# Performance work log

Measured on AMD Instinct MI355X. Metric: run time of the kernel, lower is better.

The kernel has to match this reference:

```python
import jax, jax.numpy as jnp
import numpy as np

B, M, T, L, K = 64, 16, 2048, 64, 32
N = T - L + 1  # 1985 sliding-window positions


def setup_inputs() -> dict:
    key = jax.random.key(0)
    k1, k2, k3 = jax.random.split(key, 3)
    x = jax.random.normal(k1, (B, M, T), dtype=jnp.float32)
    # shapelets initialized uniform(-1, 1) as in nn.init.uniform_
    shapelets = jax.random.uniform(k2, (K, L), dtype=jnp.float32, minval=-1.0, maxval=1.0)
    # penalty maps (learned; zeros at init, random here for a non-trivial weighting)
    penalty_maps = 0.1 * jax.random.normal(k3, (K, M, N), dtype=jnp.float32)
    return {"x": x, "shapelets": shapelets, "penalty_maps": penalty_maps}


def reference(x, shapelets, penalty_maps):
    # x: (B, M, T); shapelets: (K, L); penalty_maps: (K, M, N)
    Lw = shapelets.shape[1]
    n_pos = x.shape[2] - Lw + 1
    # sliding-window view: (B, M, N, L), equivalent to torch unfold(dim=2, size=L, step=1)
    idx = jnp.arange(n_pos)[:, None] + jnp.arange(Lw)[None, :]
    sub = x[:, :, idx]  # (B, M, N, L)

    def per_shapelet(args):
        shp, pmap = args  # (L,), (M, N)
        # raw squared L2 distance over window, per channel/position: (B, M, N)
        raw = jnp.sum((sub - shp[None, None, None, :]) ** 2, axis=3)
        pen = jax.nn.elu(-pmap) + 2.0  # (M, N)
        wd = jnp.sum(raw * pen[None], axis=1)  # sum over channels -> (B, N)
        return jnp.min(wd, axis=1)  # min over positions -> (B,)

    # sequential map over the K shapelets avoids a Kx blow-up of the (B,M,N,L) intermediate
    feats = jax.lax.map(per_shapelet, (shapelets, penalty_maps))  # (K, B)
    return feats.T  # (B, K)
```

## Files before the change

kernel.cpp:

```cpp
#include <hip/hip_runtime.h>
#include <hip/hip_bf16.h>

#define B_ 64
#define M_ 16
#define T_ 2048
#define L_ 64
#define K_ 32
#define N_ (T_ - L_ + 1)
#define KMN (K_ * M_ * N_)
#define TN 64
#define NTH 256
#define XROW 128
#define STSTR 72
#define SQSTR 68

typedef __attribute__((ext_vector_type(8))) short bf16x8;
typedef __attribute__((ext_vector_type(4))) float f32x4;

__device__ __forceinline__ unsigned short f2bf(float f) {
    __hip_bfloat16 h = __float2bfloat16(f);
    return __builtin_bit_cast(unsigned short, h);
}

__device__ __forceinline__ unsigned funnel16(unsigned lo, unsigned hi, unsigned sh) {
    return (unsigned)(((((unsigned long long)hi) << 32) | lo) >> sh);
}

__device__ __forceinline__ bf16x8 extract_frag(uint4 a, uint4 b, unsigned sh, int c2) {
    unsigned t0 = funnel16(a.x, a.y, sh), t1 = funnel16(a.y, a.z, sh);
    unsigned t2 = funnel16(a.z, a.w, sh), t3 = funnel16(a.w, b.x, sh);
    unsigned t4 = funnel16(b.x, b.y, sh), t5 = funnel16(b.y, b.z, sh);
    unsigned t6 = funnel16(b.z, b.w, sh);
    const bool s2 = (c2 & 2), s1 = (c2 & 1);
    unsigned u0 = s2 ? t2 : t0, u1 = s2 ? t3 : t1, u2 = s2 ? t4 : t2;
    unsigned u3 = s2 ? t5 : t3, u4 = s2 ? t6 : t4;
    union { unsigned u[4]; bf16x8 v; } cvt;
    cvt.u[0] = s1 ? u1 : u0; cvt.u[1] = s1 ? u2 : u1;
    cvt.u[2] = s1 ? u3 : u2; cvt.u[3] = s1 ? u4 : u3;
    return cvt.v;
}

__global__ void pen_init_kernel(const float* __restrict__ pmap,
                                float* __restrict__ pen,
                                unsigned* __restrict__ out) {
    const int gid = blockIdx.x * 256 + threadIdx.x;
    if (gid < B_ * K_) out[gid] = 0x7F800000u;
    if (gid < KMN / 4) {
        const int i4 = gid * 4;
        float4 p = *(const float4*)(pmap + i4);
        float4 r;
        r.x = (p.x < 0.f) ? (2.f - p.x) : (__expf(-p.x) + 1.f);
        r.y = (p.y < 0.f) ? (2.f - p.y) : (__expf(-p.y) + 1.f);
        r.z = (p.z < 0.f) ? (2.f - p.z) : (__expf(-p.z) + 1.f);
        r.w = (p.w < 0.f) ? (2.f - p.w) : (__expf(-p.w) + 1.f);
        *(float4*)(pen + i4) = r;
    }
}

__global__ __launch_bounds__(NTH, 2)
void shapelet_mfma_kernel(const float* __restrict__ x,
                          const float* __restrict__ shp,
                          const float* __restrict__ pen,
                          unsigned* __restrict__ out) {
    __shared__ __align__(16) unsigned short xbuf[M_][XROW];
    __shared__ __align__(16) unsigned short st[K_][STSTR];
    __shared__ __align__(16) float sqw[M_][SQSTR];
    __shared__ float ss_l[K_];

    const int tid = threadIdx.x;
    const int n0 = blockIdx.x * TN;
    const int b  = blockIdx.y;
    const bool fast = (n0 + TN < T_);

    const float* xb = x + ((size_t)b * M_) * T_ + n0;
    for (int g = tid; g < M_ * 32; g += NTH) {
        const int m = g >> 5, j4 = (g & 31) * 4;
        const float* src = xb + m * T_ + j4;
        float4 v;
        if (fast) {
            v = *(const float4*)src;
        } else {
            v = make_float4(0.f, 0.f, 0.f, 0.f);
            const int t = n0 + j4;
            if (t     < T_) v.x = src[0];
            if (t + 1 < T_) v.y = src[1];
            if (t + 2 < T_) v.z = src[2];
            if (t + 3 < T_) v.w = src[3];
        }
        ushort4 sv = { f2bf(v.x), f2bf(v.y), f2bf(v.z), f2bf(v.w) };
        *(ushort4*)&xbuf[m][j4] = sv;
    }
    for (int i = tid; i < K_ * 16; i += NTH) {
        const int k = i >> 4, l4 = (i & 15) * 4;
        float4 v = *(const float4*)(shp + k * L_ + l4);
        ushort4 sv = { f2bf(v.x), f2bf(v.y), f2bf(v.z), f2bf(v.w) };
        *(ushort4*)&st[k][l4] = sv;
    }
    if (tid < K_) {
        float s = 0.f;
        for (int l = 0; l < L_; ++l) { float v = shp[tid * L_ + l]; s = fmaf(v, v, s); }
        ss_l[tid] = s;
    }
    if (tid < M_ * 8) {
        const int m = tid >> 3, j0 = (tid & 7) * 8;
        const float* xr = x + ((size_t)b * M_ + m) * T_ + n0;
        float s = 0.f;
        if (fast) {
#pragma unroll
            for (int qd = 0; qd < 16; ++qd) {
                float4 v = *(const float4*)(xr + j0 + qd * 4);
                s = fmaf(v.x, v.x, s); s = fmaf(v.y, v.y, s);
                s = fmaf(v.z, v.z, s); s = fmaf(v.w, v.w, s);
            }
            sqw[m][j0] = s;
#pragma unroll
            for (int d = 1; d < 8; ++d) {
                float a = xr[j0 + d + L_ - 1], r = xr[j0 + d - 1];
                s += a * a - r * r;
                sqw[m][j0 + d] = s;
            }
        } else {
            for (int l = 0; l < L_; ++l) {
                float v = (n0 + j0 + l < T_) ? xr[j0 + l] : 0.f;
                s = fmaf(v, v, s);
            }
            sqw[m][j0] = s;
            for (int d = 1; d < 8; ++d) {
                float a = (n0 + j0 + d + L_ - 1 < T_) ? xr[j0 + d + L_ - 1] : 0.f;
                float r = (n0 + j0 + d - 1 < T_) ? xr[j0 + d - 1] : 0.f;
                s += a * a - r * r;
                sqw[m][j0 + d] = s;
            }
        }
    }
    __syncthreads();

    const int lane = tid & 63;
    const int w  = tid >> 6;
    const int rl = lane & 15;
    const int q  = lane >> 4;
    const int rho = rl & 7, r8 = rl >> 3;
    const unsigned sh = (unsigned)((rho & 1) * 16);
    const int c2 = rho >> 1;
    const int Gb = 2 * w + q + r8;

    bf16x8 bfr[2][2];
#pragma unroll
    for (int t = 0; t < 2; ++t)
#pragma unroll
        for (int h = 0; h < 2; ++h)
            bfr[t][h] = *(const bf16x8*)&st[16 * t + rl][8 * q + 32 * h];

    const float ssk0 = ss_l[rl], ssk1 = ss_l[16 + rl];

    f32x4 wd0 = (f32x4)0.f, wd1 = (f32x4)0.f;
    const int nrow = n0 + 16 * w + 4 * q;
    const f32x4 zero = (f32x4)0.f;

#pragma unroll 2
    for (int m = 0; m < M_; ++m) {
        float4 p0, p1;
        const float* pr0 = pen + ((size_t)(rl * M_ + m)) * N_ + nrow;
        const float* pr1 = pen + ((size_t)((16 + rl) * M_ + m)) * N_ + nrow;
        if (fast) {
            p0 = *(const float4*)pr0;
            p1 = *(const float4*)pr1;
        } else {
            p0 = make_float4(2.f, 2.f, 2.f, 2.f);
            p1 = make_float4(2.f, 2.f, 2.f, 2.f);
            if (nrow     < N_) { p0.x = pr0[0]; p1.x = pr1[0]; }
            if (nrow + 1 < N_) { p0.y = pr0[1]; p1.y = pr1[1]; }
            if (nrow + 2 < N_) { p0.z = pr0[2]; p1.z = pr1[2]; }
            if (nrow + 3 < N_) { p0.w = pr0[3]; p1.w = pr1[3]; }
        }

        const uint4* px = (const uint4*)&xbuf[m][0];
        uint4 w0 = px[Gb],     w1 = px[Gb + 1];
        uint4 w2 = px[Gb + 4], w3 = px[Gb + 5];
        bf16x8 a0 = extract_frag(w0, w1, sh, c2);
        bf16x8 a1 = extract_frag(w2, w3, sh, c2);

        f32x4 corr0 = __builtin_amdgcn_mfma_f32_16x16x32_bf16(a0, bfr[0][0], zero, 0, 0, 0);
        corr0       = __builtin_amdgcn_mfma_f32_16x16x32_bf16(a1, bfr[0][1], corr0, 0, 0, 0);
        f32x4 corr1 = __builtin_amdgcn_mfma_f32_16x16x32_bf16(a0, bfr[1][0], zero, 0, 0, 0);
        corr1       = __builtin_amdgcn_mfma_f32_16x16x32_bf16(a1, bfr[1][1], corr1, 0, 0, 0);

        f32x4 sq = *(const f32x4*)&sqw[m][16 * w + 4 * q];
        const float pe0[4] = { p0.x, p0.y, p0.z, p0.w };
        const float pe1[4] = { p1.x, p1.y, p1.z, p1.w };
#pragma unroll
        for (int r = 0; r < 4; ++r) {
            float t0v = fmaf(-2.f, corr0[r], sq[r] + ssk0);
            wd0[r] = fmaf(pe0[r], t0v, wd0[r]);
            float t1v = fmaf(-2.f, corr1[r], sq[r] + ssk1);
            wd1[r] = fmaf(pe1[r], t1v, wd1[r]);
        }
    }

#pragma unroll
    for (int t = 0; t < 2; ++t) {
        float lmin = __int_as_float(0x7F800000);
        const f32x4& wdv = t ? wd1 : wd0;
#pragma unroll
        for (int r = 0; r < 4; ++r) {
            if (nrow + r < N_) lmin = fminf(lmin, wdv[r]);
        }
        lmin = fminf(lmin, __shfl_xor(lmin, 16));
        lmin = fminf(lmin, __shfl_xor(lmin, 32));
        if (q == 0) {
            atomicMin(out + (size_t)b * K_ + 16 * t + rl,
                      __float_as_uint(fmaxf(lmin, 0.f)));
        }
    }
}

extern "C" void kernel_launch(void* const* d_in, const int* in_sizes, int n_in,
                              void* d_out, int out_size, void* d_ws, size_t ws_size,
                              hipStream_t stream) {
    const float* x    = (const float*)d_in[0];
    const float* shp  = (const float*)d_in[1];
    const float* pmap = (const float*)d_in[2];
    unsigned* out = (unsigned*)d_out;
    float* pen = (float*)d_ws;

    pen_init_kernel<<<dim3((KMN / 4 + 255) / 256), dim3(256), 0, stream>>>(pmap, pen, out);

    dim3 grid((N_ + TN - 1) / TN, B_);
    shapelet_mfma_kernel<<<grid, dim3(NTH), 0, stream>>>(x, shp, pen, out);
}
```

Baseline: 106.0 us.

## Prefetch penalty loads ahead, precompute shapelet norms, reduce atomics via shared memory

Penalty-map loads are software-pipelined, with two channel iterations prefetched into registers ahead of compute. The first loads are issued before the staging phase so global latency overlaps the x/shapelet conversion. Shapelet squared norms move into the init kernel and are stored in workspace instead of being computed serially by 32 threads in every block. Per-wave minima are combined in shared memory so each block issues 32 atomics instead of 128. The cost is more register pressure from the prefetch buffers and one extra barrier.

```diff
diff --git a/kernel.cpp b/kernel.cpp
--- a/kernel.cpp
+++ b/kernel.cpp
@@ -41,10 +41,17 @@
 }
 
 __global__ void pen_init_kernel(const float* __restrict__ pmap,
+                                const float* __restrict__ shp,
                                 float* __restrict__ pen,
+                                float* __restrict__ ss_ws,
                                 unsigned* __restrict__ out) {
     const int gid = blockIdx.x * 256 + threadIdx.x;
     if (gid < B_ * K_) out[gid] = 0x7F800000u;
+    if (gid < K_) {
+        float s = 0.f;
+        for (int l = 0; l < L_; ++l) { float v = shp[gid * L_ + l]; s = fmaf(v, v, s); }
+        ss_ws[gid] = s;
+    }
     if (gid < KMN / 4) {
         const int i4 = gid * 4;
         float4 p = *(const float4*)(pmap + i4);
@@ -61,16 +68,53 @@
 void shapelet_mfma_kernel(const float* __restrict__ x,
                           const float* __restrict__ shp,
                           const float* __restrict__ pen,
+                          const float* __restrict__ ss_ws,
                           unsigned* __restrict__ out) {
     __shared__ __align__(16) unsigned short xbuf[M_][XROW];
     __shared__ __align__(16) unsigned short st[K_][STSTR];
     __shared__ __align__(16) float sqw[M_][SQSTR];
-    __shared__ float ss_l[K_];
+    __shared__ float red[4][2][16];
 
     const int tid = threadIdx.x;
     const int n0 = blockIdx.x * TN;
     const int b  = blockIdx.y;
     const bool fast = (n0 + TN < T_);
+
+    const int lane = tid & 63;
+    const int w  = tid >> 6;
+    const int rl = lane & 15;
+    const int q  = lane >> 4;
+    const int rho = rl & 7, r8 = rl >> 3;
+    const unsigned sh = (unsigned)((rho & 1) * 16);
+    const int c2 = rho >> 1;
+    const int Gb = 2 * w + q + r8;
+    const int nrow = n0 + 16 * w + 4 * q;
+
+    const float* pb0 = pen + (size_t)rl * (M_ * N_) + nrow;
+    const float* pb1 = pb0 + (size_t)16 * M_ * N_;
+
+#define PEN_LOAD(mi, P0, P1) do {                                              \
+        if (fast) {                                                            \
+            P0 = *(const float4*)(pb0 + (size_t)(mi) * N_);                    \
+            P1 = *(const float4*)(pb1 + (size_t)(mi) * N_);                    \
+        } else {                                                               \
+            P0 = make_float4(2.f, 2.f, 2.f, 2.f);                              \
+            P1 = make_float4(2.f, 2.f, 2.f, 2.f);                              \
+            const float* r0_ = pb0 + (size_t)(mi) * N_;                        \
+            const float* r1_ = pb1 + (size_t)(mi) * N_;                        \
+            if (nrow     < N_) { P0.x = r0_[0]; P1.x = r1_[0]; }               \
+            if (nrow + 1 < N_) { P0.y = r0_[1]; P1.y = r1_[1]; }               \
+            if (nrow + 2 < N_) { P0.z = r0_[2]; P1.z = r1_[2]; }               \
+            if (nrow + 3 < N_) { P0.w = r0_[3]; P1.w = r1_[3]; }               \
+        }                                                                      \
+    } while (0)
+
+    float4 pf0[4], pf1[4];
+    PEN_LOAD(0, pf0[0], pf1[0]);
+    PEN_LOAD(1, pf0[1], pf1[1]);
+    PEN_LOAD(2, pf0[2], pf1[2]);
+    PEN_LOAD(3, pf0[3], pf1[3]);
+    const float ssk0 = ss_ws[rl], ssk1 = ss_ws[16 + rl];
 
     const float* xb = x + ((size_t)b * M_) * T_ + n0;
     for (int g = tid; g < M_ * 32; g += NTH) {
@@ -96,11 +140,6 @@
         ushort4 sv = { f2bf(v.x), f2bf(v.y), f2bf(v.z), f2bf(v.w) };
         *(ushort4*)&st[k][l4] = sv;
     }
-    if (tid < K_) {
-        float s = 0.f;
-        for (int l = 0; l < L_; ++l) { float v = shp[tid * L_ + l]; s = fmaf(v, v, s); }
-        ss_l[tid] = s;
-    }
     if (tid < M_ * 8) {
         const int m = tid >> 3, j0 = (tid & 7) * 8;
         const float* xr = x + ((size_t)b * M_ + m) * T_ + n0;
@@ -135,15 +174,6 @@
     }
     __syncthreads();
 
-    const int lane = tid & 63;
-    const int w  = tid >> 6;
-    const int rl = lane & 15;
-    const int q  = lane >> 4;
-    const int rho = rl & 7, r8 = rl >> 3;
-    const unsigned sh = (unsigned)((rho & 1) * 16);
-    const int c2 = rho >> 1;
-    const int Gb = 2 * w + q + r8;
-
     bf16x8 bfr[2][2];
 #pragma unroll
     for (int t = 0; t < 2; ++t)
@@ -151,50 +181,43 @@
         for (int h = 0; h < 2; ++h)
             bfr[t][h] = *(const bf16x8*)&st[16 * t + rl][8 * q + 32 * h];
 
-    const float ssk0 = ss_l[rl], ssk1 = ss_l[16 + rl];
-
     f32x4 wd0 = (f32x4)0.f, wd1 = (f32x4)0.f;
-    const int nrow = n0 + 16 * w + 4 * q;
     const f32x4 zero = (f32x4)0.f;
 
-#pragma unroll 2
-    for (int m = 0; m < M_; ++m) {
-        float4 p0, p1;
-        const float* pr0 = pen + ((size_t)(rl * M_ + m)) * N_ + nrow;
-        const float* pr1 = pen + ((size_t)((16 + rl) * M_ + m)) * N_ + nrow;
-        if (fast) {
-            p0 = *(const float4*)pr0;
-            p1 = *(const float4*)pr1;
-        } else {
-            p0 = make_float4(2.f, 2.f, 2.f, 2.f);
-            p1 = make_float4(2.f, 2.f, 2.f, 2.f);
-            if (nrow     < N_) { p0.x = pr0[0]; p1.x = pr1[0]; }
-            if (nrow + 1 < N_) { p0.y = pr0[1]; p1.y = pr1[1]; }
-            if (nrow + 2 < N_) { p0.z = pr0[2]; p1.z = pr1[2]; }
-            if (nrow + 3 < N_) { p0.w = pr0[3]; p1.w = pr1[3]; }
-        }
-
-        const uint4* px = (const uint4*)&xbuf[m][0];
-        uint4 w0 = px[Gb],     w1 = px[Gb + 1];
-        uint4 w2 = px[Gb + 4], w3 = px[Gb + 5];
-        bf16x8 a0 = extract_frag(w0, w1, sh, c2);
-        bf16x8 a1 = extract_frag(w2, w3, sh, c2);
-
-        f32x4 corr0 = __builtin_amdgcn_mfma_f32_16x16x32_bf16(a0, bfr[0][0], zero, 0, 0, 0);
-        corr0       = __builtin_amdgcn_mfma_f32_16x16x32_bf16(a1, bfr[0][1], corr0, 0, 0, 0);
-        f32x4 corr1 = __builtin_amdgcn_mfma_f32_16x16x32_bf16(a0, bfr[1][0], zero, 0, 0, 0);
-        corr1       = __builtin_amdgcn_mfma_f32_16x16x32_bf16(a1, bfr[1][1], corr1, 0, 0, 0);
-
-        f32x4 sq = *(const f32x4*)&sqw[m][16 * w + 4 * q];
-        const float pe0[4] = { p0.x, p0.y, p0.z, p0.w };
-        const float pe1[4] = { p1.x, p1.y, p1.z, p1.w };
-#pragma unroll
-        for (int r = 0; r < 4; ++r) {
-            float t0v = fmaf(-2.f, corr0[r], sq[r] + ssk0);
-            wd0[r] = fmaf(pe0[r], t0v, wd0[r]);
-            float t1v = fmaf(-2.f, corr1[r], sq[r] + ssk1);
-            wd1[r] = fmaf(pe1[r], t1v, wd1[r]);
-        }
+#define COMPUTE_M(mi, P0, P1) do {                                             \
+        const uint4* px = (const uint4*)&xbuf[mi][0];                          \
+        uint4 w0_ = px[Gb],     w1_ = px[Gb + 1];                              \
+        uint4 w2_ = px[Gb + 4], w3_ = px[Gb + 5];                              \
+        bf16x8 A0 = extract_frag(w0_, w1_, sh, c2);                            \
+        bf16x8 A1 = extract_frag(w2_, w3_, sh, c2);                            \
+        f32x4 c0_ = __builtin_amdgcn_mfma_f32_16x16x32_bf16(A0, bfr[0][0], zero, 0, 0, 0); \
+        c0_       = __builtin_amdgcn_mfma_f32_16x16x32_bf16(A1, bfr[0][1], c0_, 0, 0, 0);  \
+        f32x4 c1_ = __builtin_amdgcn_mfma_f32_16x16x32_bf16(A0, bfr[1][0], zero, 0, 0, 0); \
+        c1_       = __builtin_amdgcn_mfma_f32_16x16x32_bf16(A1, bfr[1][1], c1_, 0, 0, 0);  \
+        f32x4 sq_ = *(const f32x4*)&sqw[mi][16 * w + 4 * q];                   \
+        const float pe0_[4] = { P0.x, P0.y, P0.z, P0.w };                      \
+        const float pe1_[4] = { P1.x, P1.y, P1.z, P1.w };                      \
+        _Pragma("unroll")                                                      \
+        for (int r = 0; r < 4; ++r) {                                          \
+            float t0v = fmaf(-2.f, c0_[r], sq_[r] + ssk0);                     \
+            wd0[r] = fmaf(pe0_[r], t0v, wd0[r]);                               \
+            float t1v = fmaf(-2.f, c1_[r], sq_[r] + ssk1);                     \
+            wd1[r] = fmaf(pe1_[r], t1v, wd1[r]);                               \
+        }                                                                      \
+    } while (0)
+
+#pragma unroll 1
+    for (int mm = 0; mm < M_; mm += 2) {
+        float4 q00 = pf0[0], q01 = pf1[0];
+        float4 q10 = pf0[1], q11 = pf1[1];
+        pf0[0] = pf0[2]; pf1[0] = pf1[2];
+        pf0[1] = pf0[3]; pf1[1] = pf1[3];
+        if (mm + 5 < M_) {
+            PEN_LOAD(mm + 4, pf0[2], pf1[2]);
+            PEN_LOAD(mm + 5, pf0[3], pf1[3]);
+        }
+        COMPUTE_M(mm,     q00, q01);
+        COMPUTE_M(mm + 1, q10, q11);
     }
 
 #pragma unroll
@@ -207,11 +230,17 @@
         }
         lmin = fminf(lmin, __shfl_xor(lmin, 16));
         lmin = fminf(lmin, __shfl_xor(lmin, 32));
-        if (q == 0) {
-            atomicMin(out + (size_t)b * K_ + 16 * t + rl,
-                      __float_as_uint(fmaxf(lmin, 0.f)));
-        }
-    }
+        if (q == 0) red[w][t][rl] = lmin;
+    }
+    __syncthreads();
+    if (tid < K_) {
+        const int t = tid >> 4, kr = tid & 15;
+        float v = fminf(fminf(red[0][t][kr], red[1][t][kr]),
+                        fminf(red[2][t][kr], red[3][t][kr]));
+        atomicMin(out + (size_t)b * K_ + tid, __float_as_uint(fmaxf(v, 0.f)));
+    }
+#undef PEN_LOAD
+#undef COMPUTE_M
 }
 
 extern "C" void kernel_launch(void* const* d_in, const int* in_sizes, int n_in,
@@ -221,10 +250,12 @@
     const float* shp  = (const float*)d_in[1];
     const float* pmap = (const float*)d_in[2];
     unsigned* out = (unsigned*)d_out;
-    float* pen = (float*)d_ws;
-
-    pen_init_kernel<<<dim3((KMN / 4 + 255) / 256), dim3(256), 0, stream>>>(pmap, pen, out);
+    float* pen   = (float*)d_ws;
+    float* ss_ws = pen + KMN;
+
+    pen_init_kernel<<<dim3((KMN / 4 + 255) / 256), dim3(256), 0, stream>>>(
+        pmap, shp, pen, ss_ws, out);
 
     dim3 grid((N_ + TN - 1) / TN, B_);
-    shapelet_mfma_kernel<<<grid, dim3(NTH), 0, stream>>>(x, shp, pen, out);
-}
+    shapelet_mfma_kernel<<<grid, dim3(NTH), 0, stream>>>(x, shp, pen, ss_ws, out);
+}
```

Measured after the change: 115.2 us. 1.09x slower.

## Store four shifted bf16 copies of x in LDS to skip funnel-shift fragment extraction

Applied to the files above, without the earlier changes.

Builds four copies of each channel's bf16 x row in shared memory, each shifted by one element. An MFMA A-fragment then comes straight from aligned 8-byte loads instead of per-iteration funnel shifts and selects. The shapelet squared-norm computation also moves from every block into the pen_init kernel, with the result stored in the workspace. The cost is four times the LDS footprint for x and extra global traffic during staging.

```diff
diff --git a/kernel.cpp b/kernel.cpp
--- a/kernel.cpp
+++ b/kernel.cpp
@@ -10,9 +10,9 @@
 #define KMN (K_ * M_ * N_)
 #define TN 64
 #define NTH 256
-#define XROW 128
+#define XROW 144
 #define STSTR 72
-#define SQSTR 68
+#define SQSTR 64
 
 typedef __attribute__((ext_vector_type(8))) short bf16x8;
 typedef __attribute__((ext_vector_type(4))) float f32x4;
@@ -22,29 +22,18 @@
     return __builtin_bit_cast(unsigned short, h);
 }
 
-__device__ __forceinline__ unsigned funnel16(unsigned lo, unsigned hi, unsigned sh) {
-    return (unsigned)(((((unsigned long long)hi) << 32) | lo) >> sh);
-}
-
-__device__ __forceinline__ bf16x8 extract_frag(uint4 a, uint4 b, unsigned sh, int c2) {
-    unsigned t0 = funnel16(a.x, a.y, sh), t1 = funnel16(a.y, a.z, sh);
-    unsigned t2 = funnel16(a.z, a.w, sh), t3 = funnel16(a.w, b.x, sh);
-    unsigned t4 = funnel16(b.x, b.y, sh), t5 = funnel16(b.y, b.z, sh);
-    unsigned t6 = funnel16(b.z, b.w, sh);
-    const bool s2 = (c2 & 2), s1 = (c2 & 1);
-    unsigned u0 = s2 ? t2 : t0, u1 = s2 ? t3 : t1, u2 = s2 ? t4 : t2;
-    unsigned u3 = s2 ? t5 : t3, u4 = s2 ? t6 : t4;
-    union { unsigned u[4]; bf16x8 v; } cvt;
-    cvt.u[0] = s1 ? u1 : u0; cvt.u[1] = s1 ? u2 : u1;
-    cvt.u[2] = s1 ? u3 : u2; cvt.u[3] = s1 ? u4 : u3;
-    return cvt.v;
-}
-
 __global__ void pen_init_kernel(const float* __restrict__ pmap,
+                                const float* __restrict__ shp,
                                 float* __restrict__ pen,
+                                float* __restrict__ ss_ws,
                                 unsigned* __restrict__ out) {
     const int gid = blockIdx.x * 256 + threadIdx.x;
     if (gid < B_ * K_) out[gid] = 0x7F800000u;
+    if (gid < K_) {
+        float s = 0.f;
+        for (int l = 0; l < L_; ++l) { float v = shp[gid * L_ + l]; s = fmaf(v, v, s); }
+        ss_ws[gid] = s;
+    }
     if (gid < KMN / 4) {
         const int i4 = gid * 4;
         float4 p = *(const float4*)(pmap + i4);
@@ -61,45 +50,46 @@
 void shapelet_mfma_kernel(const float* __restrict__ x,
                           const float* __restrict__ shp,
                           const float* __restrict__ pen,
+                          const float* __restrict__ ss_ws,
                           unsigned* __restrict__ out) {
-    __shared__ __align__(16) unsigned short xbuf[M_][XROW];
+    __shared__ __align__(16) unsigned short xbuf4[M_][4][XROW];
     __shared__ __align__(16) unsigned short st[K_][STSTR];
     __shared__ __align__(16) float sqw[M_][SQSTR];
-    __shared__ float ss_l[K_];
 
     const int tid = threadIdx.x;
     const int n0 = blockIdx.x * TN;
     const int b  = blockIdx.y;
-    const bool fast = (n0 + TN < T_);
+    const bool fast = (n0 + 128 <= T_);
 
     const float* xb = x + ((size_t)b * M_) * T_ + n0;
-    for (int g = tid; g < M_ * 32; g += NTH) {
-        const int m = g >> 5, j4 = (g & 31) * 4;
+    for (int g = tid; g < M_ * 31; g += NTH) {
+        const int m = g / 31, j4 = (g - m * 31) * 4;
         const float* src = xb + m * T_ + j4;
-        float4 v;
+        float h[8];
         if (fast) {
-            v = *(const float4*)src;
+            float4 v0 = *(const float4*)src;
+            float4 v1 = *(const float4*)(src + 4);
+            h[0] = v0.x; h[1] = v0.y; h[2] = v0.z; h[3] = v0.w;
+            h[4] = v1.x; h[5] = v1.y; h[6] = v1.z; h[7] = v1.w;
         } else {
-            v = make_float4(0.f, 0.f, 0.f, 0.f);
-            const int t = n0 + j4;
-            if (t     < T_) v.x = src[0];
-            if (t + 1 < T_) v.y = src[1];
-            if (t + 2 < T_) v.z = src[2];
-            if (t + 3 < T_) v.w = src[3];
-        }
-        ushort4 sv = { f2bf(v.x), f2bf(v.y), f2bf(v.z), f2bf(v.w) };
-        *(ushort4*)&xbuf[m][j4] = sv;
+#pragma unroll
+            for (int i = 0; i < 8; ++i)
+                h[i] = (n0 + j4 + i < T_) ? src[i] : 0.f;
+        }
+        unsigned short hb[8];
+#pragma unroll
+        for (int i = 0; i < 8; ++i) hb[i] = f2bf(h[i]);
+#pragma unroll
+        for (int s = 0; s < 4; ++s) {
+            ushort4 sv = { hb[s], hb[s + 1], hb[s + 2], hb[s + 3] };
+            *(ushort4*)&xbuf4[m][s][j4] = sv;
+        }
     }
     for (int i = tid; i < K_ * 16; i += NTH) {
         const int k = i >> 4, l4 = (i & 15) * 4;
         float4 v = *(const float4*)(shp + k * L_ + l4);
         ushort4 sv = { f2bf(v.x), f2bf(v.y), f2bf(v.z), f2bf(v.w) };
         *(ushort4*)&st[k][l4] = sv;
-    }
-    if (tid < K_) {
-        float s = 0.f;
-        for (int l = 0; l < L_; ++l) { float v = shp[tid * L_ + l]; s = fmaf(v, v, s); }
-        ss_l[tid] = s;
     }
     if (tid < M_ * 8) {
         const int m = tid >> 3, j0 = (tid & 7) * 8;
@@ -139,10 +129,10 @@
     const int w  = tid >> 6;
     const int rl = lane & 15;
     const int q  = lane >> 4;
-    const int rho = rl & 7, r8 = rl >> 3;
-    const unsigned sh = (unsigned)((rho & 1) * 16);
-    const int c2 = rho >> 1;
-    const int Gb = 2 * w + q + r8;
+    const int sp = rl & 3;
+    const int e0 = 16 * w + 8 * q + (rl & ~3);
+    const int eq = e0 >> 2;
+    const int nrow = n0 + 16 * w + 4 * q;
 
     bf16x8 bfr[2][2];
 #pragma unroll
@@ -151,48 +141,51 @@
         for (int h = 0; h < 2; ++h)
             bfr[t][h] = *(const bf16x8*)&st[16 * t + rl][8 * q + 32 * h];
 
-    const float ssk0 = ss_l[rl], ssk1 = ss_l[16 + rl];
+    const float ssk0 = ss_ws[rl], ssk1 = ss_ws[16 + rl];
+
+    const float* pr0 = pen + (size_t)rl * (M_ * N_) + nrow;
+    const float* pr1 = pr0 + (size_t)16 * M_ * N_;
 
     f32x4 wd0 = (f32x4)0.f, wd1 = (f32x4)0.f;
-    const int nrow = n0 + 16 * w + 4 * q;
     const f32x4 zero = (f32x4)0.f;
 
 #pragma unroll 2
     for (int m = 0; m < M_; ++m) {
         float4 p0, p1;
-        const float* pr0 = pen + ((size_t)(rl * M_ + m)) * N_ + nrow;
-        const float* pr1 = pen + ((size_t)((16 + rl) * M_ + m)) * N_ + nrow;
         if (fast) {
-            p0 = *(const float4*)pr0;
-            p1 = *(const float4*)pr1;
+            p0 = *(const float4*)(pr0 + (size_t)m * N_);
+            p1 = *(const float4*)(pr1 + (size_t)m * N_);
         } else {
             p0 = make_float4(2.f, 2.f, 2.f, 2.f);
             p1 = make_float4(2.f, 2.f, 2.f, 2.f);
-            if (nrow     < N_) { p0.x = pr0[0]; p1.x = pr1[0]; }
-            if (nrow + 1 < N_) { p0.y = pr0[1]; p1.y = pr1[1]; }
-            if (nrow + 2 < N_) { p0.z = pr0[2]; p1.z = pr1[2]; }
-            if (nrow + 3 < N_) { p0.w = pr0[3]; p1.w = pr1[3]; }
-        }
-
-        const uint4* px = (const uint4*)&xbuf[m][0];
-        uint4 w0 = px[Gb],     w1 = px[Gb + 1];
-        uint4 w2 = px[Gb + 4], w3 = px[Gb + 5];
-        bf16x8 a0 = extract_frag(w0, w1, sh, c2);
-        bf16x8 a1 = extract_frag(w2, w3, sh, c2);
-
-        f32x4 corr0 = __builtin_amdgcn_mfma_f32_16x16x32_bf16(a0, bfr[0][0], zero, 0, 0, 0);
-        corr0       = __builtin_amdgcn_mfma_f32_16x16x32_bf16(a1, bfr[0][1], corr0, 0, 0, 0);
-        f32x4 corr1 = __builtin_amdgcn_mfma_f32_16x16x32_bf16(a0, bfr[1][0], zero, 0, 0, 0);
-        corr1       = __builtin_amdgcn_mfma_f32_16x16x32_bf16(a1, bfr[1][1], corr1, 0, 0, 0);
+            const float* r0_ = pr0 + (size_t)m * N_;
+            const float* r1_ = pr1 + (size_t)m * N_;
+            if (nrow     < N_) { p0.x = r0_[0]; p1.x = r1_[0]; }
+            if (nrow + 1 < N_) { p0.y = r0_[1]; p1.y = r1_[1]; }
+            if (nrow + 2 < N_) { p0.z = r0_[2]; p1.z = r1_[2]; }
+            if (nrow + 3 < N_) { p0.w = r0_[3]; p1.w = r1_[3]; }
+        }
+
+        const uint2* prow = (const uint2*)&xbuf4[m][sp][0];
+        uint2 lo0 = prow[eq],     hi0 = prow[eq + 1];
+        uint2 lo1 = prow[eq + 8], hi1 = prow[eq + 9];
+        union { uint2 u2[2]; bf16x8 v; } fa0, fa1;
+        fa0.u2[0] = lo0; fa0.u2[1] = hi0;
+        fa1.u2[0] = lo1; fa1.u2[1] = hi1;
+
+        f32x4 c0_ = __builtin_amdgcn_mfma_f32_16x16x32_bf16(fa0.v, bfr[0][0], zero, 0, 0, 0);
+        c0_       = __builtin_amdgcn_mfma_f32_16x16x32_bf16(fa1.v, bfr[0][1], c0_, 0, 0, 0);
+        f32x4 c1_ = __builtin_amdgcn_mfma_f32_16x16x32_bf16(fa0.v, bfr[1][0], zero, 0, 0, 0);
+        c1_       = __builtin_amdgcn_mfma_f32_16x16x32_bf16(fa1.v, bfr[1][1], c1_, 0, 0, 0);
 
         f32x4 sq = *(const f32x4*)&sqw[m][16 * w + 4 * q];
         const float pe0[4] = { p0.x, p0.y, p0.z, p0.w };
         const float pe1[4] = { p1.x, p1.y, p1.z, p1.w };
 #pragma unroll
         for (int r = 0; r < 4; ++r) {
-            float t0v = fmaf(-2.f, corr0[r], sq[r] + ssk0);
+            float t0v = fmaf(-2.f, c0_[r], sq[r] + ssk0);
             wd0[r] = fmaf(pe0[r], t0v, wd0[r]);
-            float t1v = fmaf(-2.f, corr1[r], sq[r] + ssk1);
+            float t1v = fmaf(-2.f, c1_[r], sq[r] + ssk1);
             wd1[r] = fmaf(pe1[r], t1v, wd1[r]);
         }
     }
@@ -221,10 +214,12 @@
     const float* shp  = (const float*)d_in[1];
     const float* pmap = (const float*)d_in[2];
     unsigned* out = (unsigned*)d_out;
-    float* pen = (float*)d_ws;
-
-    pen_init_kernel<<<dim3((KMN / 4 + 255) / 256), dim3(256), 0, stream>>>(pmap, pen, out);
+    float* pen   = (float*)d_ws;
+    float* ss_ws = pen + KMN;
+
+    pen_init_kernel<<<dim3((KMN / 4 + 255) / 256), dim3(256), 0, stream>>>(
+        pmap, shp, pen, ss_ws, out);
 
     dim3 grid((N_ + TN - 1) / TN, B_);
-    shapelet_mfma_kernel<<<grid, dim3(NTH), 0, stream>>>(x, shp, pen, out);
-}
+    shapelet_mfma_kernel<<<grid, dim3(NTH), 0, stream>>>(x, shp, pen, ss_ws, out);
+}
```

After: 100.9 us. -4.7%, faster.
